# Optimization experiments

Hardware: AMD Instinct MI355X
Metric: run time of the kernel (lower is better)

The kernel has to match this reference:

```python
import jax, jax.numpy as jnp
import numpy as np

N = 100000      # nodes
E = 3200000     # edges (avg degree 32)
D = 256         # feature dim
C = 40          # classes
KEEP = 0.5      # 1 - dropout


def setup_inputs() -> dict:
    key = jax.random.key(0)
    k1, k2, k3, k4, k5, k6, k7 = jax.random.split(key, 7)
    x = jax.random.normal(k1, (N, D), dtype=jnp.float32)
    adj_row = jnp.sort(jax.random.randint(k2, (E,), 0, N))
    adj_col = jax.random.randint(k3, (E,), 0, N)
    # roughly degree-normalized edge weights (~1/avg_degree scale)
    adj_vals = jax.random.uniform(k4, (E,), dtype=jnp.float32) * (2.0 / 32.0)
    W = jax.random.normal(k5, (C, D), dtype=jnp.float32) * (1.0 / np.sqrt(D))
    b = jax.random.normal(k6, (C,), dtype=jnp.float32) * 0.01
    # precomputed dropout keep-mask (training mode, p=0.5)
    drop_mask = (jax.random.uniform(k7, (N, D)) < KEEP).astype(jnp.float32)
    return {"x": x, "adj_vals": adj_vals, "W": W, "b": b,
            "drop_mask": drop_mask, "adj_row": adj_row, "adj_col": adj_col}


def reference(x, adj_vals, W, b, drop_mask, adj_row, adj_col):
    n = x.shape[0]

    def spmm(v):  # sparse [N,N] @ dense [N,d] via gather + segment-sum
        return jax.ops.segment_sum(adj_vals[:, None] * v[adj_col], adj_row,
                                   num_segments=n)

    # hidden GraphConvolution (use_linear=False): spmm -> relu -> dropout
    h = jax.nn.relu(spmm(x))
    h = h * drop_mask / KEEP
    # gc_class: Linear(D->C) then spmm
    out = spmm(h @ W.T + b)  # [N, C]
    return out
```

## Files before the change

kernel.cpp:

```cpp
#include <hip/hip_runtime.h>

#define NN 100000
#define EE 3200000
#define DD 256
#define CC 40
#define NCH 8
#define CH 32
#define UN2 8

#define CAP 2432
#define ROWS_PB 64
#define COHORT 256
#define CHUNK_BLOCKS (COHORT * 8)
#define RG64 1563
#define LROWS 64

__device__ __forceinline__ float bf2f(unsigned int u) {
    return __uint_as_float(u << 16);
}
__device__ __forceinline__ unsigned short f2bf(float f) {
    unsigned int t = __float_as_uint(f);
    return (unsigned short)((t + 0x7FFFu + ((t >> 16) & 1u)) >> 16);
}

__global__ __launch_bounds__(256) void k_row_ptr(const int* __restrict__ adj_row,
                                                 int* __restrict__ row_ptr) {
    int e = blockIdx.x * 256 + threadIdx.x;
    if (e >= EE) return;
    int r = adj_row[e];
    int prev = (e == 0) ? -1 : adj_row[e - 1];
    for (int rr = prev + 1; rr <= r; ++rr) row_ptr[rr] = e;
    if (e == EE - 1) {
        for (int rr = r + 1; rr <= NN; ++rr) row_ptr[rr] = EE;
    }
}

__global__ __launch_bounds__(256) void k_cvt_t(const float* __restrict__ x,
                                               ushort* __restrict__ xb) {
    __shared__ ushort ls[32][DD + 4];
    int t = threadIdx.x;
    size_t r0 = (size_t)blockIdx.x * 32;
    const float4* src = (const float4*)(x + r0 * DD);
#pragma unroll
    for (int u = 0; u < 8; ++u) {
        int idx = u * 256 + t;
        float4 v = src[idx];
        int row = idx >> 6, d4 = idx & 63;
        ushort* p = &ls[row][d4 * 4];
        p[0] = f2bf(v.x); p[1] = f2bf(v.y); p[2] = f2bf(v.z); p[3] = f2bf(v.w);
    }
    __syncthreads();
    int c = t >> 5, r = t & 31;
    const uint4* s = (const uint4*)&ls[r][c * CH];
    uint4* dst = (uint4*)(xb + ((size_t)c * NN + r0 + r) * CH);
    dst[0] = s[0];
    dst[1] = s[1];
    dst[2] = s[2];
    dst[3] = s[3];
}

__global__ __launch_bounds__(256, 7) void k_chunk(
    const ushort* __restrict__ xb, const float* __restrict__ adj_vals,
    const int* __restrict__ adj_col, const int* __restrict__ row_ptr,
    const float* __restrict__ drop_mask, ushort* __restrict__ hb)
{
    __shared__ uint2 meta[CAP + 8];
    int bid = blockIdx.x;
    int c = bid & 7;
    int q = bid >> 3;
    int wave = threadIdx.x >> 6, lane = threadIdx.x & 63;
    int g = lane >> 2, i = lane & 3;
    const ushort* xc = xb + (size_t)c * NN * CH;

    for (int rg = q; rg < RG64; rg += COHORT) {
        int row0 = rg * ROWS_PB;
        int row  = row0 + wave * 16 + g;
        bool rv  = row < NN;
        int rend = min(row0 + ROWS_PB, NN);
        int e_start = __builtin_amdgcn_readfirstlane(row_ptr[row0]);
        int e_end   = __builtin_amdgcn_readfirstlane(row_ptr[rend]);
        int nstage  = min(e_end - e_start, CAP);

        for (int t = threadIdx.x; t < nstage; t += 256) {
            uint2 m;
            m.x = (unsigned)adj_col[e_start + t];
            m.y = __float_as_uint(adj_vals[e_start + t]);
            meta[t] = m;
        }
        __syncthreads();

        int e0  = rv ? row_ptr[row] : 0;
        int cnt = rv ? row_ptr[row + 1] - e0 : 0;
        int eloc = e0 - e_start;
        float a0 = 0.f, a1 = 0.f, a2 = 0.f, a3 = 0.f;
        float a4 = 0.f, a5 = 0.f, a6 = 0.f, a7 = 0.f;

        if (eloc + cnt <= nstage) {
            int body = cnt & ~(UN2 - 1);
            int k = 0;
            for (; k < body; k += UN2) {
                uint2 mm[UN2];
#pragma unroll
                for (int u = 0; u < UN2; ++u) mm[u] = meta[eloc + k + u];
                uint4 xv[UN2];
#pragma unroll
                for (int u = 0; u < UN2; ++u)
                    xv[u] = *(const uint4*)(xc + (size_t)mm[u].x * CH + i * 8);
#pragma unroll
                for (int u = 0; u < UN2; ++u) {
                    float v = __uint_as_float(mm[u].y);
                    a0 = fmaf(v, bf2f(xv[u].x & 0xFFFFu), a0);
                    a1 = fmaf(v, bf2f(xv[u].x >> 16),     a1);
                    a2 = fmaf(v, bf2f(xv[u].y & 0xFFFFu), a2);
                    a3 = fmaf(v, bf2f(xv[u].y >> 16),     a3);
                    a4 = fmaf(v, bf2f(xv[u].z & 0xFFFFu), a4);
                    a5 = fmaf(v, bf2f(xv[u].z >> 16),     a5);
                    a6 = fmaf(v, bf2f(xv[u].w & 0xFFFFu), a6);
                    a7 = fmaf(v, bf2f(xv[u].w >> 16),     a7);
                }
            }
            if (k < cnt) {
#pragma unroll
                for (int u = 0; u < UN2; ++u) {
                    int kk = k + u;
                    uint2 m = meta[eloc + min(kk, cnt - 1)];
                    float v = (kk < cnt) ? __uint_as_float(m.y) : 0.f;
                    uint4 xv = *(const uint4*)(xc + (size_t)m.x * CH + i * 8);
                    a0 = fmaf(v, bf2f(xv.x & 0xFFFFu), a0);
                    a1 = fmaf(v, bf2f(xv.x >> 16),     a1);
                    a2 = fmaf(v, bf2f(xv.y & 0xFFFFu), a2);
                    a3 = fmaf(v, bf2f(xv.y >> 16),     a3);
                    a4 = fmaf(v, bf2f(xv.z & 0xFFFFu), a4);
                    a5 = fmaf(v, bf2f(xv.z >> 16),     a5);
                    a6 = fmaf(v, bf2f(xv.w & 0xFFFFu), a6);
                    a7 = fmaf(v, bf2f(xv.w >> 16),     a7);
                }
            }
        } else {
            for (int k = 0; k < cnt; ++k) {
                int idx = e0 + k;
                float v = adj_vals[idx];
                int col = adj_col[idx];
                uint4 xv = *(const uint4*)(xc + (size_t)col * CH + i * 8);
                a0 = fmaf(v, bf2f(xv.x & 0xFFFFu), a0);
                a1 = fmaf(v, bf2f(xv.x >> 16),     a1);
                a2 = fmaf(v, bf2f(xv.y & 0xFFFFu), a2);
                a3 = fmaf(v, bf2f(xv.y >> 16),     a3);
                a4 = fmaf(v, bf2f(xv.z & 0xFFFFu), a4);
                a5 = fmaf(v, bf2f(xv.z >> 16),     a5);
                a6 = fmaf(v, bf2f(xv.w & 0xFFFFu), a6);
                a7 = fmaf(v, bf2f(xv.w >> 16),     a7);
            }
        }
        __syncthreads();

        if (rv) {
            size_t off = (size_t)row * DD + c * CH + i * 8;
            const float* mp = drop_mask + off;
            float m0 = __builtin_nontemporal_load(mp);
            float m1 = __builtin_nontemporal_load(mp + 1);
            float m2 = __builtin_nontemporal_load(mp + 2);
            float m3 = __builtin_nontemporal_load(mp + 3);
            float m4 = __builtin_nontemporal_load(mp + 4);
            float m5 = __builtin_nontemporal_load(mp + 5);
            float m6 = __builtin_nontemporal_load(mp + 6);
            float m7 = __builtin_nontemporal_load(mp + 7);
            float h0 = fmaxf(a0, 0.f) * m0 * 2.f;
            float h1 = fmaxf(a1, 0.f) * m1 * 2.f;
            float h2 = fmaxf(a2, 0.f) * m2 * 2.f;
            float h3 = fmaxf(a3, 0.f) * m3 * 2.f;
            float h4 = fmaxf(a4, 0.f) * m4 * 2.f;
            float h5 = fmaxf(a5, 0.f) * m5 * 2.f;
            float h6 = fmaxf(a6, 0.f) * m6 * 2.f;
            float h7 = fmaxf(a7, 0.f) * m7 * 2.f;
            unsigned long long p0 =
                (unsigned long long)((unsigned)f2bf(h0) | ((unsigned)f2bf(h1) << 16)) |
                ((unsigned long long)((unsigned)f2bf(h2) | ((unsigned)f2bf(h3) << 16)) << 32);
            unsigned long long p1 =
                (unsigned long long)((unsigned)f2bf(h4) | ((unsigned)f2bf(h5) << 16)) |
                ((unsigned long long)((unsigned)f2bf(h6) | ((unsigned)f2bf(h7) << 16)) << 32);
            __builtin_nontemporal_store(p0, (unsigned long long*)(hb + off));
            __builtin_nontemporal_store(p1, (unsigned long long*)(hb + off + 4));
        }
    }
}

__global__ __launch_bounds__(256) void k_linear(
    const ushort* __restrict__ hb, const float* __restrict__ W,
    const float* __restrict__ b, float* __restrict__ z)
{
    __shared__ float ws[CC][DD + 4];
    int t = threadIdx.x;
    for (int idx = t; idx < CC * (DD / 4); idx += 256) {
        int c = idx >> 6, k4 = idx & 63;
        float4 v = ((const float4*)(W + (size_t)c * DD))[k4];
        float* p = &ws[c][k4 * 4];
        p[0] = v.x; p[1] = v.y; p[2] = v.z; p[3] = v.w;
    }
    __syncthreads();

    int row = blockIdx.x * LROWS + (t >> 2);
    int cg = (t & 3) * 10;
    if (row >= NN) return;

    const uint4* hrow = (const uint4*)(hb + (size_t)row * DD);
    float acc[10] = {0.f, 0.f, 0.f, 0.f, 0.f, 0.f, 0.f, 0.f, 0.f, 0.f};

    for (int k8 = 0; k8 < DD / 8; ++k8) {
        uint4 hv = hrow[k8];
        float h0 = bf2f(hv.x & 0xFFFFu), h1 = bf2f(hv.x >> 16);
        float h2 = bf2f(hv.y & 0xFFFFu), h3 = bf2f(hv.y >> 16);
        float h4 = bf2f(hv.z & 0xFFFFu), h5 = bf2f(hv.z >> 16);
        float h6 = bf2f(hv.w & 0xFFFFu), h7 = bf2f(hv.w >> 16);
#pragma unroll
        for (int j = 0; j < 10; ++j) {
            const float* wp = &ws[cg + j][k8 * 8];
            float4 wa = *(const float4*)wp;
            float4 wb = *(const float4*)(wp + 4);
            acc[j] = fmaf(h0, wa.x, fmaf(h1, wa.y,
                     fmaf(h2, wa.z, fmaf(h3, wa.w, acc[j]))));
            acc[j] = fmaf(h4, wb.x, fmaf(h5, wb.y,
                     fmaf(h6, wb.z, fmaf(h7, wb.w, acc[j]))));
        }
    }
#pragma unroll
    for (int j = 0; j < 10; ++j)
        z[(size_t)row * CC + cg + j] = acc[j] + b[cg + j];
}

__global__ __launch_bounds__(256) void k_spmm2(
    const float* __restrict__ z, const float* __restrict__ adj_vals,
    const int* __restrict__ adj_col, const int* __restrict__ row_ptr,
    float* __restrict__ out)
{
    int wave = threadIdx.x >> 6;
    int lane = threadIdx.x & 63;
    int row = blockIdx.x * 4 + wave;
    int cl = lane < CC ? lane : CC - 1;

    int e0 = __builtin_amdgcn_readfirstlane(row_ptr[row]);
    int e1 = __builtin_amdgcn_readfirstlane(row_ptr[row + 1]);

    float acc = 0.f;
    int nb = (e1 - e0 + UN2 - 1) / UN2;
    for (int bI = 0; bI < nb; ++bI) {
        int base = e0 + bI * UN2;
        float vv[UN2]; int cc[UN2];
#pragma unroll
        for (int u = 0; u < UN2; ++u) {
            int idx = base + u;
            bool ok = idx < e1;
            idx = ok ? idx : e1 - 1;
            vv[u] = ok ? adj_vals[idx] : 0.f;
            cc[u] = adj_col[idx];
        }
        float za[UN2];
#pragma unroll
        for (int u = 0; u < UN2; ++u)
            za[u] = z[(size_t)cc[u] * CC + cl];
#pragma unroll
        for (int u = 0; u < UN2; ++u)
            acc = fmaf(vv[u], za[u], acc);
    }
    if (lane < CC) out[(size_t)row * CC + lane] = acc;
}

extern "C" void kernel_launch(void* const* d_in, const int* in_sizes, int n_in,
                              void* d_out, int out_size, void* d_ws, size_t ws_size,
                              hipStream_t stream) {
    const float* x         = (const float*)d_in[0];
    const float* adj_vals  = (const float*)d_in[1];
    const float* W         = (const float*)d_in[2];
    const float* b         = (const float*)d_in[3];
    const float* drop_mask = (const float*)d_in[4];
    const int*   adj_row   = (const int*)d_in[5];
    const int*   adj_col   = (const int*)d_in[6];
    float* out = (float*)d_out;

    char* wsp = (char*)d_ws;
    size_t rp_bytes = ((size_t)(NN + 1) * 4 + 255) & ~(size_t)255;
    size_t z_bytes  = (size_t)NN * CC * 4;
    size_t xb_bytes = (size_t)NN * DD * 2;
    int* row_ptr = (int*)wsp;
    float* zbuf  = (float*)(wsp + rp_bytes);
    ushort* xb   = (ushort*)(wsp + rp_bytes + z_bytes);
    ushort* hb   = (ushort*)(wsp + rp_bytes + z_bytes + xb_bytes);

    hipLaunchKernelGGL(k_row_ptr, dim3((EE + 255) / 256), dim3(256), 0, stream,
                       adj_row, row_ptr);
    hipLaunchKernelGGL(k_cvt_t, dim3(NN / 32), dim3(256), 0, stream, x, xb);
    hipLaunchKernelGGL(k_chunk, dim3(CHUNK_BLOCKS), dim3(256), 0, stream,
                       xb, adj_vals, adj_col, row_ptr, drop_mask, hb);
    hipLaunchKernelGGL(k_linear, dim3((NN + LROWS - 1) / LROWS), dim3(256), 0,
                       stream, hb, W, b, zbuf);
    hipLaunchKernelGGL(k_spmm2, dim3(NN / 4), dim3(256), 0, stream,
                       zbuf, adj_vals, adj_col, row_ptr, out);
}
```

Before: 465.9 us.

## Make k_chunk per-wave with private LDS staging and store z in bf16

```diff
diff --git a/kernel.cpp b/kernel.cpp
--- a/kernel.cpp
+++ b/kernel.cpp
@@ -8,11 +8,11 @@
 #define CH 32
 #define UN2 8
 
-#define CAP 2432
-#define ROWS_PB 64
+#define CAPW 640
 #define COHORT 256
 #define CHUNK_BLOCKS (COHORT * 8)
-#define RG64 1563
+#define WPC (COHORT * 4)
+#define WG16 (NN / 16)
 #define LROWS 64
 
 __device__ __forceinline__ float bf2f(unsigned int u) {
@@ -59,38 +59,39 @@
     dst[3] = s[3];
 }
 
-__global__ __launch_bounds__(256, 7) void k_chunk(
+__global__ __launch_bounds__(256, 8) void k_chunk(
     const ushort* __restrict__ xb, const float* __restrict__ adj_vals,
     const int* __restrict__ adj_col, const int* __restrict__ row_ptr,
     const float* __restrict__ drop_mask, ushort* __restrict__ hb)
 {
-    __shared__ uint2 meta[CAP + 8];
+    __shared__ uint2 meta[4][CAPW];
     int bid = blockIdx.x;
     int c = bid & 7;
     int q = bid >> 3;
     int wave = threadIdx.x >> 6, lane = threadIdx.x & 63;
     int g = lane >> 2, i = lane & 3;
     const ushort* xc = xb + (size_t)c * NN * CH;
-
-    for (int rg = q; rg < RG64; rg += COHORT) {
-        int row0 = rg * ROWS_PB;
-        int row  = row0 + wave * 16 + g;
-        bool rv  = row < NN;
-        int rend = min(row0 + ROWS_PB, NN);
+    uint2* mw = meta[wave];
+    int gw0 = q * 4 + wave;
+
+    for (int wg = gw0; wg < WG16; wg += WPC) {
+        int row0 = wg * 16;
+        int row  = row0 + g;
         int e_start = __builtin_amdgcn_readfirstlane(row_ptr[row0]);
-        int e_end   = __builtin_amdgcn_readfirstlane(row_ptr[rend]);
-        int nstage  = min(e_end - e_start, CAP);
-
-        for (int t = threadIdx.x; t < nstage; t += 256) {
+        int e_end   = __builtin_amdgcn_readfirstlane(row_ptr[row0 + 16]);
+        int nstage  = min(e_end - e_start, CAPW);
+
+        for (int t = lane; t < nstage; t += 64) {
             uint2 m;
             m.x = (unsigned)adj_col[e_start + t];
             m.y = __float_as_uint(adj_vals[e_start + t]);
-            meta[t] = m;
-        }
-        __syncthreads();
-
-        int e0  = rv ? row_ptr[row] : 0;
-        int cnt = rv ? row_ptr[row + 1] - e0 : 0;
+            mw[t] = m;
+        }
+        asm volatile("s_waitcnt lgkmcnt(0)" ::: "memory");
+        __builtin_amdgcn_wave_barrier();
+
+        int e0  = row_ptr[row];
+        int cnt = row_ptr[row + 1] - e0;
         int eloc = e0 - e_start;
         float a0 = 0.f, a1 = 0.f, a2 = 0.f, a3 = 0.f;
         float a4 = 0.f, a5 = 0.f, a6 = 0.f, a7 = 0.f;
@@ -101,7 +102,7 @@
             for (; k < body; k += UN2) {
                 uint2 mm[UN2];
 #pragma unroll
-                for (int u = 0; u < UN2; ++u) mm[u] = meta[eloc + k + u];
+                for (int u = 0; u < UN2; ++u) mm[u] = mw[eloc + k + u];
                 uint4 xv[UN2];
 #pragma unroll
                 for (int u = 0; u < UN2; ++u)
@@ -123,7 +124,7 @@
 #pragma unroll
                 for (int u = 0; u < UN2; ++u) {
                     int kk = k + u;
-                    uint2 m = meta[eloc + min(kk, cnt - 1)];
+                    uint2 m = mw[eloc + min(kk, cnt - 1)];
                     float v = (kk < cnt) ? __uint_as_float(m.y) : 0.f;
                     uint4 xv = *(const uint4*)(xc + (size_t)m.x * CH + i * 8);
                     a0 = fmaf(v, bf2f(xv.x & 0xFFFFu), a0);
@@ -152,9 +153,9 @@
                 a7 = fmaf(v, bf2f(xv.w >> 16),     a7);
             }
         }
-        __syncthreads();
-
-        if (rv) {
+        __builtin_amdgcn_wave_barrier();
+
+        {
             size_t off = (size_t)row * DD + c * CH + i * 8;
             const float* mp = drop_mask + off;
             float m0 = __builtin_nontemporal_load(mp);
@@ -187,7 +188,7 @@
 
 __global__ __launch_bounds__(256) void k_linear(
     const ushort* __restrict__ hb, const float* __restrict__ W,
-    const float* __restrict__ b, float* __restrict__ z)
+    const float* __restrict__ b, ushort* __restrict__ z)
 {
     __shared__ float ws[CC][DD + 4];
     int t = threadIdx.x;
@@ -225,11 +226,11 @@
     }
 #pragma unroll
     for (int j = 0; j < 10; ++j)
-        z[(size_t)row * CC + cg + j] = acc[j] + b[cg + j];
+        z[(size_t)row * CC + cg + j] = f2bf(acc[j] + b[cg + j]);
 }
 
 __global__ __launch_bounds__(256) void k_spmm2(
-    const float* __restrict__ z, const float* __restrict__ adj_vals,
+    const ushort* __restrict__ z, const float* __restrict__ adj_vals,
     const int* __restrict__ adj_col, const int* __restrict__ row_ptr,
     float* __restrict__ out)
 {
@@ -257,7 +258,7 @@
         float za[UN2];
 #pragma unroll
         for (int u = 0; u < UN2; ++u)
-            za[u] = z[(size_t)cc[u] * CC + cl];
+            za[u] = bf2f((unsigned)z[(size_t)cc[u] * CC + cl]);
 #pragma unroll
         for (int u = 0; u < UN2; ++u)
             acc = fmaf(vv[u], za[u], acc);
@@ -282,7 +283,7 @@
     size_t z_bytes  = (size_t)NN * CC * 4;
     size_t xb_bytes = (size_t)NN * DD * 2;
     int* row_ptr = (int*)wsp;
-    float* zbuf  = (float*)(wsp + rp_bytes);
+    ushort* zbuf = (ushort*)(wsp + rp_bytes);
     ushort* xb   = (ushort*)(wsp + rp_bytes + z_bytes);
     ushort* hb   = (ushort*)(wsp + rp_bytes + z_bytes + xb_bytes);
 
```

Result: faster. 445.2 us (-4.4%).
